# Kernel optimization log

Measured on AMD Instinct MI355X. Metric: run time of the kernel, lower is better.

## Reference

```python
import jax, jax.numpy as jnp
import numpy as np
from jax import lax

B = 1024
D_VQ = 64
KS = 1024
KX = 1024
BETA = 0.25


def _conv1d(x, w, b):
    # x: [N, Cin, L], w: [Cout, Cin, 3], 'same' padding
    y = lax.conv_general_dilated(x, w, (1,), [(1, 1)], dimension_numbers=('NCH', 'OIH', 'NCH'))
    return y + b[None, :, None]


def _conv2d(x, w, b):
    # x: [N, Cin, H, W], w: [Cout, Cin, 3, 3], 'same' padding
    y = lax.conv_general_dilated(x, w, (1, 1), [(1, 1), (1, 1)], dimension_numbers=('NCHW', 'OIHW', 'NCHW'))
    return y + b[None, :, None, None]


def _gelu(x):
    return jax.nn.gelu(x, approximate=False)


def _vq_ema(z_e, codebook, beta):
    # z_e: [N, D], codebook: [K, D]
    d = (jnp.sum(z_e * z_e, axis=1, keepdims=True)
         - 2.0 * (z_e @ codebook.T)
         + jnp.sum(codebook * codebook, axis=1)[None, :])  # [N, K]
    idx = jnp.argmin(d, axis=1)                              # [N]
    z_q = codebook[idx]                                      # gather [N, D]
    vq_loss = beta * jnp.mean((z_e - lax.stop_gradient(z_q)) ** 2)
    z_q_st = z_e + lax.stop_gradient(z_q - z_e)              # straight-through
    n = z_e.shape[0]
    probs = jnp.zeros((codebook.shape[0],), z_e.dtype).at[idx].add(1.0) / n
    perplexity = jnp.exp(-jnp.sum(probs * jnp.log(probs + 1e-10)))
    return z_q_st, idx, vq_loss, perplexity


def setup_inputs() -> dict:
    key = jax.random.key(0)
    ks = iter(jax.random.split(key, 40))

    def p(shape, s=0.05):
        return jax.random.normal(next(ks), shape, jnp.float32) * s

    inp = {
        'cubes': jax.random.normal(next(ks), (B, 9, 8, 72), jnp.float32),
        # spectral encoder
        's_w1': p((16, 1, 3)), 's_b1': jnp.zeros((16,), jnp.float32),
        's_w2': p((16, 16, 3)), 's_b2': jnp.zeros((16,), jnp.float32),
        's_fc_w': p((D_VQ, 16 * 8)), 's_fc_b': jnp.zeros((D_VQ,), jnp.float32),
        'cb_s': p((KS, D_VQ), 1.0),
        # spectral decoder
        's_dec_fc_w': p((16 * 8, D_VQ)), 's_dec_fc_b': jnp.zeros((16 * 8,), jnp.float32),
        's_dec_w1': p((16, 16, 3)), 's_dec_b1': jnp.zeros((16,), jnp.float32),
        's_dec_w2': p((1, 16, 3)), 's_dec_b2': jnp.zeros((1,), jnp.float32),
        # spatial encoder
        'x_w1': p((16, 8, 3, 3)), 'x_b1': jnp.zeros((16,), jnp.float32),
        'x_w2': p((16, 16, 3, 3)), 'x_b2': jnp.zeros((16,), jnp.float32),
        'x_fc_w': p((D_VQ, 16 * 3 * 3)), 'x_fc_b': jnp.zeros((D_VQ,), jnp.float32),
        'cb_x': p((KX, D_VQ), 1.0),
        # spatial decoder
        'x_dec_fc_w': p((16 * 3 * 3, D_VQ)), 'x_dec_fc_b': jnp.zeros((16 * 3 * 3,), jnp.float32),
        'x_dec_w1': p((16, 16, 3, 3)), 'x_dec_b1': jnp.zeros((16,), jnp.float32),
        'x_dec_w2': p((8, 16, 3, 3)), 'x_dec_b2': jnp.zeros((8,), jnp.float32),
        'return_recon': 1,
    }
    return inp


def reference(cubes, s_w1, s_b1, s_w2, s_b2, s_fc_w, s_fc_b, cb_s,
              s_dec_fc_w, s_dec_fc_b, s_dec_w1, s_dec_b1, s_dec_w2, s_dec_b2,
              x_w1, x_b1, x_w2, x_b2, x_fc_w, x_fc_b, cb_x,
              x_dec_fc_w, x_dec_fc_b, x_dec_w1, x_dec_b1, x_dec_w2, x_dec_b2,
              return_recon):
    b, p, t, f = cubes.shape
    n = b * p * t
    c6 = cubes.reshape(b, p, t, 8, 3, 3)                   # [B,P,T,8,3,3]
    cperm = jnp.transpose(c6, (0, 1, 2, 4, 5, 3))          # [B,P,T,3,3,8]

    # --- spectral path ---
    spec = jnp.mean(cperm, axis=(3, 4))                    # [B,P,T,8]
    spec_seq = spec.reshape(n, 1, 8)
    s = _gelu(_conv1d(spec_seq, s_w1, s_b1))
    s = _gelu(_conv1d(s, s_w2, s_b2))
    z_e_s = s.reshape(n, 16 * 8) @ s_fc_w.T + s_fc_b       # [N,D]
    z_q_s, k_idx, vq_loss_s, perplex_s = _vq_ema(z_e_s, cb_s, BETA)
    emb_s = z_q_s.reshape(b, p, t, D_VQ)
    k_idx = k_idx.reshape(b, p, t)

    # --- spatial path ---
    spatial = c6.reshape(n, 8, 3, 3)
    x = _gelu(_conv2d(spatial, x_w1, x_b1))
    x = _gelu(_conv2d(x, x_w2, x_b2))
    z_e_x = x.reshape(n, 16 * 9) @ x_fc_w.T + x_fc_b
    z_q_x, m_idx, vq_loss_x, perplex_x = _vq_ema(z_e_x, cb_x, BETA)
    emb_x = z_q_x.reshape(b, p, t, D_VQ)
    m_idx = m_idx.reshape(b, p, t)

    total = vq_loss_s + vq_loss_x

    if return_recon:
        s_dec = (z_q_s @ s_dec_fc_w.T + s_dec_fc_b).reshape(n, 16, 8)
        s_dec = _gelu(_conv1d(s_dec, s_dec_w1, s_dec_b1))
        recon_s = _conv1d(s_dec, s_dec_w2, s_dec_b2)[:, 0, :].reshape(b, p, t, 8)
        recon_loss_s = jnp.mean((recon_s - spec) ** 2)

        x_dec = (z_q_x @ x_dec_fc_w.T + x_dec_fc_b).reshape(n, 16, 3, 3)
        x_dec = _gelu(_conv2d(x_dec, x_dec_w1, x_dec_b1))
        recon_x = _conv2d(x_dec, x_dec_w2, x_dec_b2)        # [N,8,3,3]
        recon_loss_x = jnp.mean((recon_x - spatial) ** 2)
        recon_loss_total = recon_loss_s + recon_loss_x
    else:
        recon_loss_total = jnp.float32(0.0)

    return (emb_s, emb_x, k_idx, m_idx, total, perplex_s, perplex_x, recon_loss_total)
```

## Files before the change

kernel.cpp:

```cpp
#include <hip/hip_runtime.h>
#include <math.h>

#define NTOK 73728

__device__ __forceinline__ float gelu_f(float x) {
    return 0.5f * x * (1.0f + erff(x * 0.70710678118654752440f));
}

__global__ void __launch_bounds__(256) k_prep(
    const float* __restrict__ cb_s, const float* __restrict__ cb_x,
    double* __restrict__ cn_s, double* __restrict__ cn_x,
    const float* __restrict__ s_dw1, const float* __restrict__ s_db1,
    const float* __restrict__ s_dfcw, const float* __restrict__ s_dfcb,
    float* __restrict__ weffT_s, float* __restrict__ beff_s,
    const float* __restrict__ x_dw1, const float* __restrict__ x_db1,
    const float* __restrict__ x_dfcw, const float* __restrict__ x_dfcb,
    float* __restrict__ weffT_x, float* __restrict__ beff_x,
    const float* __restrict__ s_fcw, float* __restrict__ fcwT_s,
    const float* __restrict__ x_fcw, float* __restrict__ fcwT_x,
    const float* __restrict__ s_w2, float* __restrict__ sw2T,
    const float* __restrict__ x_w1, float* __restrict__ xw1T,
    const float* __restrict__ x_w2, float* __restrict__ xw2T,
    const float* __restrict__ x_dw2, float* __restrict__ xdw2T)
{
    int bid = blockIdx.x, tid = threadIdx.x;
    if (bid < 8) {
        int i = bid * 256 + tid;
        const float* cb = (i < 1024) ? cb_s : cb_x;
        double* cn = (i < 1024) ? cn_s : cn_x;
        int c = i & 1023;
        double s = 0.0;
        for (int k = 0; k < 64; ++k) { double v = (double)cb[c * 64 + k]; s += v * v; }
        cn[c] = s;
    } else if (bid < 40) {
        int idx = (bid - 8) * 256 + tid;
        int o = idx >> 6, d = idx & 63;
        int c = o >> 3, l = o & 7;
        double acc = 0.0;
        for (int ci = 0; ci < 16; ++ci)
            for (int dd = 0; dd < 3; ++dd) {
                int ll = l + dd - 1;
                if (ll < 0 || ll > 7) continue;
                acc += (double)s_dw1[(c * 16 + ci) * 3 + dd] * (double)s_dfcw[(ci * 8 + ll) * 64 + d];
            }
        weffT_s[d * 132 + o] = (float)acc;
        if (o < 4) weffT_s[d * 132 + 128 + o] = 0.f;
        if (d == 0) {
            double bb = (double)s_db1[c];
            for (int ci = 0; ci < 16; ++ci)
                for (int dd = 0; dd < 3; ++dd) {
                    int ll = l + dd - 1;
                    if (ll < 0 || ll > 7) continue;
                    bb += (double)s_dw1[(c * 16 + ci) * 3 + dd] * (double)s_dfcb[ci * 8 + ll];
                }
            beff_s[o] = (float)bb;
        }
    } else if (bid < 76) {
        int idx = (bid - 40) * 256 + tid;
        int o = idx >> 6, d = idx & 63;
        int c = o / 9, p = o - c * 9;
        int i = p / 3, j = p % 3;
        double acc = 0.0;
        for (int ci = 0; ci < 16; ++ci)
            for (int di = 0; di < 3; ++di) {
                int ii = i + di - 1; if (ii < 0 || ii > 2) continue;
                for (int dj = 0; dj < 3; ++dj) {
                    int jj = j + dj - 1; if (jj < 0 || jj > 2) continue;
                    acc += (double)x_dw1[((c * 16 + ci) * 3 + di) * 3 + dj]
                         * (double)x_dfcw[(ci * 9 + ii * 3 + jj) * 64 + d];
                }
            }
        weffT_x[d * 148 + o] = (float)acc;
        if (o < 4) weffT_x[d * 148 + 144 + o] = 0.f;
        if (d == 0) {
            double bb = (double)x_db1[c];
            for (int ci = 0; ci < 16; ++ci)
                for (int di = 0; di < 3; ++di) {
                    int ii = i + di - 1; if (ii < 0 || ii > 2) continue;
                    for (int dj = 0; dj < 3; ++dj) {
                        int jj = j + dj - 1; if (jj < 0 || jj > 2) continue;
                        bb += (double)x_dw1[((c * 16 + ci) * 3 + di) * 3 + dj]
                            * (double)x_dfcb[ci * 9 + ii * 3 + jj];
                    }
                }
            beff_x[o] = (float)bb;
        }
    } else if (bid < 108) {
        int i = (bid - 76) * 256 + tid;
        fcwT_s[i] = s_fcw[(i & 63) * 128 + (i >> 6)];
    } else if (bid < 144) {
        int i = (bid - 108) * 256 + tid;
        fcwT_x[i] = x_fcw[(i & 63) * 144 + (i >> 6)];
    } else {
        int i = (bid - 144) * 256 + tid;
        if (i < 768) {
            int c = i & 15, r = i >> 4;
            int ci = r / 3, dd = r % 3;
            sw2T[i] = s_w2[(c * 16 + ci) * 3 + dd];
        } else if (i < 1920) {
            int j = i - 768;
            int c = j & 15, r = j >> 4;
            int ci = r / 9, tap = r % 9;
            xw1T[j] = x_w1[(c * 8 + ci) * 9 + tap];
        } else if (i < 4224) {
            int j = i - 1920;
            int c = j & 15, r = j >> 4;
            int ci = r / 9, tap = r % 9;
            xw2T[j] = x_w2[(c * 16 + ci) * 9 + tap];
        } else {
            int j = i - 4224;
            int co = j & 7, r = j >> 3;
            int ci = r / 9, tap = r % 9;
            xdw2T[j] = x_dw2[(co * 16 + ci) * 9 + tap];
        }
    }
}

__global__ void __launch_bounds__(256) k_enc(
    const float* __restrict__ cubes,
    const float* __restrict__ s_w1, const float* __restrict__ s_b1,
    const float* __restrict__ sw2T, const float* __restrict__ s_b2,
    const float* __restrict__ fcwT_s, const float* __restrict__ s_fcb,
    float* __restrict__ emb_s,
    const float* __restrict__ xw1T, const float* __restrict__ x_b1,
    const float* __restrict__ xw2T, const float* __restrict__ x_b2,
    const float* __restrict__ fcwT_x, const float* __restrict__ x_fcb,
    float* __restrict__ emb_x)
{
    __shared__ float U[6528];
    int tid = threadIdx.x;
    int t = tid >> 4, c = tid & 15;
    if (blockIdx.x < 4608) {
        int b = blockIdx.x;
        float* S = U;
        float* A = U + 128;
        float* Bb = U + 2304;
        if (tid < 128) {
            int tk = tid >> 3, f = tid & 7;
            const float* cu = cubes + ((size_t)b * 16 + tk) * 72 + f * 9;
            float s = 0.f;
            #pragma unroll
            for (int k = 0; k < 9; ++k) s += cu[k];
            S[tk * 8 + f] = s * (1.0f / 9.0f);
        }
        __syncthreads();
        {
            float s0[8];
            *(float4*)&s0[0] = *(const float4*)&S[t * 8];
            *(float4*)&s0[4] = *(const float4*)&S[t * 8 + 4];
            float wa = s_w1[c * 3 + 0], wb = s_w1[c * 3 + 1], wc = s_w1[c * 3 + 2], bb = s_b1[c];
            #pragma unroll
            for (int l = 0; l < 8; ++l) {
                float v = fmaf(wb, s0[l], bb);
                if (l > 0) v = fmaf(wa, s0[l - 1], v);
                if (l < 7) v = fmaf(wc, s0[l + 1], v);
                A[t * 136 + c * 8 + l] = gelu_f(v);
            }
        }
        __syncthreads();
        {
            float acc[8];
            #pragma unroll
            for (int l = 0; l < 8; ++l) acc[l] = s_b2[c];
            for (int ci = 0; ci < 16; ++ci) {
                float r[8];
                *(float4*)&r[0] = *(const float4*)&A[t * 136 + ci * 8];
                *(float4*)&r[4] = *(const float4*)&A[t * 136 + ci * 8 + 4];
                float wa = sw2T[(ci * 3 + 0) * 16 + c];
                float wb = sw2T[(ci * 3 + 1) * 16 + c];
                float wc = sw2T[(ci * 3 + 2) * 16 + c];
                #pragma unroll
                for (int l = 0; l < 8; ++l) {
                    if (l > 0) acc[l] = fmaf(wa, r[l - 1], acc[l]);
                    acc[l] = fmaf(wb, r[l], acc[l]);
                    if (l < 7) acc[l] = fmaf(wc, r[l + 1], acc[l]);
                }
            }
            #pragma unroll
            for (int l = 0; l < 8; ++l) Bb[t * 136 + c * 8 + l] = gelu_f(acc[l]);
        }
        __syncthreads();
        {
            float4 zv = make_float4(s_fcb[c * 4 + 0], s_fcb[c * 4 + 1], s_fcb[c * 4 + 2], s_fcb[c * 4 + 3]);
            #pragma unroll 4
            for (int e = 0; e < 128; ++e) {
                float be = Bb[t * 136 + e];
                float4 wv = *(const float4*)(fcwT_s + (e << 6) + (c << 2));
                zv.x = fmaf(wv.x, be, zv.x);
                zv.y = fmaf(wv.y, be, zv.y);
                zv.z = fmaf(wv.z, be, zv.z);
                zv.w = fmaf(wv.w, be, zv.w);
            }
            *(float4*)(emb_s + ((size_t)b * 16 + t) * 64 + c * 4) = zv;
        }
    } else {
        int b = blockIdx.x - 4608;
        float* A = U;
        float* Bb = U + 3200;
        for (int u = tid; u < 1152; u += 256) {
            int tk = u / 72, e = u - tk * 72;
            int ci = e / 9, p = e - ci * 9;
            A[tk * 200 + ci * 12 + p] = cubes[(size_t)b * 1152 + u];
        }
        __syncthreads();
        {
            float acc[9];
            #pragma unroll
            for (int p = 0; p < 9; ++p) acc[p] = x_b1[c];
            for (int ci = 0; ci < 8; ++ci) {
                float r[12];
                *(float4*)&r[0] = *(const float4*)&A[t * 200 + ci * 12];
                *(float4*)&r[4] = *(const float4*)&A[t * 200 + ci * 12 + 4];
                *(float4*)&r[8] = *(const float4*)&A[t * 200 + ci * 12 + 8];
                float wv[9];
                #pragma unroll
                for (int q = 0; q < 9; ++q) wv[q] = xw1T[(ci * 9 + q) * 16 + c];
                #pragma unroll
                for (int p = 0; p < 9; ++p) {
                    int i = p / 3, j = p % 3;
                    #pragma unroll
                    for (int di = 0; di < 3; ++di) {
                        int ii = i + di - 1; if (ii < 0 || ii > 2) continue;
                        #pragma unroll
                        for (int dj = 0; dj < 3; ++dj) {
                            int jj = j + dj - 1; if (jj < 0 || jj > 2) continue;
                            acc[p] = fmaf(wv[di * 3 + dj], r[ii * 3 + jj], acc[p]);
                        }
                    }
                }
            }
            #pragma unroll
            for (int p = 0; p < 9; ++p) Bb[t * 200 + c * 12 + p] = gelu_f(acc[p]);
        }
        __syncthreads();
        {
            float acc[9];
            #pragma unroll
            for (int p = 0; p < 9; ++p) acc[p] = x_b2[c];
            for (int ci = 0; ci < 16; ++ci) {
                float r[12];
                *(float4*)&r[0] = *(const float4*)&Bb[t * 200 + ci * 12];
                *(float4*)&r[4] = *(const float4*)&Bb[t * 200 + ci * 12 + 4];
                *(float4*)&r[8] = *(const float4*)&Bb[t * 200 + ci * 12 + 8];
                float wv[9];
                #pragma unroll
                for (int q = 0; q < 9; ++q) wv[q] = xw2T[(ci * 9 + q) * 16 + c];
                #pragma unroll
                for (int p = 0; p < 9; ++p) {
                    int i = p / 3, j = p % 3;
                    #pragma unroll
                    for (int di = 0; di < 3; ++di) {
                        int ii = i + di - 1; if (ii < 0 || ii > 2) continue;
                        #pragma unroll
                        for (int dj = 0; dj < 3; ++dj) {
                            int jj = j + dj - 1; if (jj < 0 || jj > 2) continue;
                            acc[p] = fmaf(wv[di * 3 + dj], r[ii * 3 + jj], acc[p]);
                        }
                    }
                }
            }
            __syncthreads();
            #pragma unroll
            for (int p = 0; p < 9; ++p) A[t * 200 + c * 12 + p] = gelu_f(acc[p]);
        }
        __syncthreads();
        {
            float4 zv = make_float4(x_fcb[c * 4 + 0], x_fcb[c * 4 + 1], x_fcb[c * 4 + 2], x_fcb[c * 4 + 3]);
            #pragma unroll 4
            for (int e = 0; e < 144; ++e) {
                int ci = e / 9, p = e - ci * 9;
                float be = A[t * 200 + ci * 12 + p];
                float4 wv = *(const float4*)(fcwT_x + (e << 6) + (c << 2));
                zv.x = fmaf(wv.x, be, zv.x);
                zv.y = fmaf(wv.y, be, zv.y);
                zv.z = fmaf(wv.z, be, zv.z);
                zv.w = fmaf(wv.w, be, zv.w);
            }
            *(float4*)(emb_x + ((size_t)b * 16 + t) * 64 + c * 4) = zv;
        }
    }
}

__global__ void __launch_bounds__(256) k_vq(
    float* __restrict__ emb_s, float* __restrict__ emb_x,
    const float* __restrict__ cb_s, const float* __restrict__ cb_x,
    const double* __restrict__ cn_s, const double* __restrict__ cn_x,
    float* __restrict__ kidx, float* __restrict__ midx,
    int* __restrict__ hist_s, int* __restrict__ hist_x,
    double* __restrict__ p_vq_s, double* __restrict__ p_vq_x)
{
    __shared__ double pbest[4][64];
    __shared__ int pidx[4][64];
    __shared__ int lh[1024];
    int blk = blockIdx.x;
    int path = (blk >= 1152) ? 1 : 0;
    int b = blk - (path << 10) - (path << 7);
    float* emb = path ? emb_x : emb_s;
    const float* cb = path ? cb_x : cb_s;
    const double* cn = path ? cn_x : cn_s;
    float* idx_out = path ? midx : kidx;
    int* hist = path ? hist_x : hist_s;
    double* partial = path ? p_vq_x : p_vq_s;

    int tid = threadIdx.x;
    int w = tid >> 6, l = tid & 63;
    for (int u = tid; u < 1024; u += 256) lh[u] = 0;
    size_t n = (size_t)b * 64 + l;
    float z[64];
    {
        const float4* zp = (const float4*)(emb + n * 64);
        #pragma unroll
        for (int k = 0; k < 16; ++k) *(float4*)&z[k * 4] = zp[k];
    }
    int base = __builtin_amdgcn_readfirstlane(w << 8);
    const float* crb = cb + ((size_t)base << 6);
    const double* cnb = cn + base;
    double best = 1e300; int bi = base;
    for (int cc = 0; cc < 256; ++cc) {
        const float* cr = crb + (cc << 6);
        float d0 = 0.f, d1 = 0.f, d2 = 0.f, d3 = 0.f;
        #pragma unroll
        for (int k = 0; k < 64; k += 4) {
            d0 = fmaf(z[k + 0], cr[k + 0], d0);
            d1 = fmaf(z[k + 1], cr[k + 1], d1);
            d2 = fmaf(z[k + 2], cr[k + 2], d2);
            d3 = fmaf(z[k + 3], cr[k + 3], d3);
        }
        float dot = (d0 + d1) + (d2 + d3);
        double dd = cnb[cc] - 2.0 * (double)dot;
        if (dd < best) { best = dd; bi = base + cc; }
    }
    pbest[w][l] = best; pidx[w][l] = bi;
    __syncthreads();
    if (w == 0) {
        double bB = pbest[0][l]; int bj = pidx[0][l];
        #pragma unroll
        for (int q = 1; q < 4; ++q) {
            double d = pbest[q][l];
            if (d < bB) { bB = d; bj = pidx[q][l]; }
        }
        idx_out[n] = (float)bj;
        float qv[64];
        {
            const float4* cq = (const float4*)(cb + ((size_t)bj << 6));
            #pragma unroll
            for (int k = 0; k < 16; ++k) *(float4*)&qv[k * 4] = cq[k];
        }
        float vs = 0.f;
        #pragma unroll
        for (int k = 0; k < 64; ++k) { float df = z[k] - qv[k]; vs = fmaf(df, df, vs); }
        float4* zo = (float4*)(emb + n * 64);
        #pragma unroll
        for (int k = 0; k < 16; ++k) zo[k] = *(float4*)&qv[k * 4];
        atomicAdd(&lh[bj], 1);
        double s = (double)vs;
        #pragma unroll
        for (int o = 32; o > 0; o >>= 1) s += __shfl_down(s, o);
        if (l == 0) partial[b] = s;
    }
    __syncthreads();
    for (int u = tid; u < 1024; u += 256) if (lh[u] > 0) atomicAdd(&hist[u], lh[u]);
}

__global__ void __launch_bounds__(256) k_dec(
    const float* __restrict__ emb_s, const float* __restrict__ emb_x,
    const float* __restrict__ cubes,
    const float* __restrict__ weffT_s, const float* __restrict__ beff_s,
    const float* __restrict__ s_dw2, const float* __restrict__ s_db2,
    const float* __restrict__ weffT_x, const float* __restrict__ beff_x,
    const float* __restrict__ xdw2T, const float* __restrict__ x_db2,
    double* __restrict__ p_rec_s, double* __restrict__ p_rec_x)
{
    __shared__ float U[6016];
    __shared__ double wred[4];
    int tid = threadIdx.x;
    int t = tid >> 4, c = tid & 15;
    if (blockIdx.x < 4608) {
        int b = blockIdx.x;
        float* Z = U;
        float* Bb = U + 1152;
        float* S = U + 3328;
        {
            int tk = tid >> 4, dq = tid & 15;
            *(float4*)&Z[tk * 72 + dq * 4] =
                *(const float4*)(emb_s + (size_t)b * 1024 + (size_t)tid * 4);
        }
        if (tid < 128) {
            int tk = tid >> 3, f = tid & 7;
            const float* cu = cubes + ((size_t)b * 16 + tk) * 72 + f * 9;
            float s = 0.f;
            #pragma unroll
            for (int k = 0; k < 9; ++k) s += cu[k];
            S[tk * 8 + f] = s * (1.0f / 9.0f);
        }
        __syncthreads();
        {
            float4 a0 = make_float4(0.f, 0.f, 0.f, 0.f);
            float4 a1 = make_float4(0.f, 0.f, 0.f, 0.f);
            #pragma unroll 8
            for (int k = 0; k < 64; ++k) {
                float zk = Z[t * 72 + k];
                float4 w0 = *(const float4*)(weffT_s + k * 132 + (c << 2));
                float4 w1v = *(const float4*)(weffT_s + k * 132 + 64 + (c << 2));
                a0.x = fmaf(w0.x, zk, a0.x); a0.y = fmaf(w0.y, zk, a0.y);
                a0.z = fmaf(w0.z, zk, a0.z); a0.w = fmaf(w0.w, zk, a0.w);
                a1.x = fmaf(w1v.x, zk, a1.x); a1.y = fmaf(w1v.y, zk, a1.y);
                a1.z = fmaf(w1v.z, zk, a1.z); a1.w = fmaf(w1v.w, zk, a1.w);
            }
            int o0 = c << 2, o1 = 64 + (c << 2);
            float4 g0 = make_float4(gelu_f(a0.x + beff_s[o0 + 0]), gelu_f(a0.y + beff_s[o0 + 1]),
                                    gelu_f(a0.z + beff_s[o0 + 2]), gelu_f(a0.w + beff_s[o0 + 3]));
            float4 g1 = make_float4(gelu_f(a1.x + beff_s[o1 + 0]), gelu_f(a1.y + beff_s[o1 + 1]),
                                    gelu_f(a1.z + beff_s[o1 + 2]), gelu_f(a1.w + beff_s[o1 + 3]));
            *(float4*)&Bb[t * 136 + o0] = g0;
            *(float4*)&Bb[t * 136 + o1] = g1;
        }
        __syncthreads();
        float acc2 = 0.f;
        {
            int h = c >> 3, pos = c & 7;
            float a = (h == 0) ? s_db2[0] : 0.f;
            for (int ci = h * 8; ci < h * 8 + 8; ++ci) {
                const float* w = s_dw2 + ci * 3;
                const float* hb = &Bb[t * 136 + ci * 8];
                if (pos > 0) a = fmaf(w[0], hb[pos - 1], a);
                a = fmaf(w[1], hb[pos], a);
                if (pos < 7) a = fmaf(w[2], hb[pos + 1], a);
            }
            a += __shfl_xor(a, 8);
            if (h == 0) { float df = a - S[t * 8 + pos]; acc2 = df * df; }
        }
        double s = (double)acc2;
        #pragma unroll
        for (int o = 32; o > 0; o >>= 1) s += __shfl_down(s, o);
        if ((tid & 63) == 0) wred[tid >> 6] = s;
        __syncthreads();
        if (tid == 0) p_rec_s[b] = wred[0] + wred[1] + wred[2] + wred[3];
    } else {
        int b = blockIdx.x - 4608;
        float* Z = U;
        float* H = U + 1152;
        float* T = U + 4352;
        {
            int tk = tid >> 4, dq = tid & 15;
            *(float4*)&Z[tk * 72 + dq * 4] =
                *(const float4*)(emb_x + (size_t)b * 1024 + (size_t)tid * 4);
        }
        for (int u = tid; u < 1152; u += 256) {
            int tk = u / 72, e = u - tk * 72;
            int ci = e / 9, p = e - ci * 9;
            T[tk * 104 + ci * 12 + p] = cubes[(size_t)b * 1152 + u];
        }
        __syncthreads();
        {
            float4 a0 = make_float4(0.f, 0.f, 0.f, 0.f);
            float4 a1 = make_float4(0.f, 0.f, 0.f, 0.f);
            float4 a2 = make_float4(0.f, 0.f, 0.f, 0.f);
            #pragma unroll 8
            for (int k = 0; k < 64; ++k) {
                float zk = Z[t * 72 + k];
                float4 w0 = *(const float4*)(weffT_x + k * 148 + (c << 2));
                float4 w1v = *(const float4*)(weffT_x + k * 148 + 64 + (c << 2));
                float4 w2v = *(const float4*)(weffT_x + k * 148 + 128 + (c << 2));
                a0.x = fmaf(w0.x, zk, a0.x); a0.y = fmaf(w0.y, zk, a0.y);
                a0.z = fmaf(w0.z, zk, a0.z); a0.w = fmaf(w0.w, zk, a0.w);
                a1.x = fmaf(w1v.x, zk, a1.x); a1.y = fmaf(w1v.y, zk, a1.y);
                a1.z = fmaf(w1v.z, zk, a1.z); a1.w = fmaf(w1v.w, zk, a1.w);
                a2.x = fmaf(w2v.x, zk, a2.x); a2.y = fmaf(w2v.y, zk, a2.y);
                a2.z = fmaf(w2v.z, zk, a2.z); a2.w = fmaf(w2v.w, zk, a2.w);
            }
            float av[12] = {a0.x, a0.y, a0.z, a0.w, a1.x, a1.y, a1.z, a1.w, a2.x, a2.y, a2.z, a2.w};
            #pragma unroll
            for (int q = 0; q < 12; ++q) {
                int o = (c << 2) + ((q >> 2) << 6) + (q & 3);
                int ch = o / 9, p = o - ch * 9;
                H[t * 200 + ch * 12 + p] = gelu_f(av[q] + beff_x[o]);
            }
        }
        __syncthreads();
        float acc2 = 0.f;
        {
            int co = c >> 1, h = c & 1;
            float accp[9];
            #pragma unroll
            for (int p = 0; p < 9; ++p) accp[p] = (h == 0) ? x_db2[co] : 0.f;
            for (int ci = h * 8; ci < h * 8 + 8; ++ci) {
                float r[12];
                *(float4*)&r[0] = *(const float4*)&H[t * 200 + ci * 12];
                *(float4*)&r[4] = *(const float4*)&H[t * 200 + ci * 12 + 4];
                *(float4*)&r[8] = *(const float4*)&H[t * 200 + ci * 12 + 8];
                float wv[9];
                #pragma unroll
                for (int q = 0; q < 9; ++q) wv[q] = xdw2T[(ci * 9 + q) * 8 + co];
                #pragma unroll
                for (int p = 0; p < 9; ++p) {
                    int i = p / 3, j = p % 3;
                    #pragma unroll
                    for (int di = 0; di < 3; ++di) {
                        int ii = i + di - 1; if (ii < 0 || ii > 2) continue;
                        #pragma unroll
                        for (int dj = 0; dj < 3; ++dj) {
                            int jj = j + dj - 1; if (jj < 0 || jj > 2) continue;
                            accp[p] = fmaf(wv[di * 3 + dj], r[ii * 3 + jj], accp[p]);
                        }
                    }
                }
            }
            #pragma unroll
            for (int p = 0; p < 9; ++p) {
                float tot = accp[p] + __shfl_xor(accp[p], 1);
                if (h == 0) { float df = tot - T[t * 104 + co * 12 + p]; acc2 = fmaf(df, df, acc2); }
            }
        }
        double s = (double)acc2;
        #pragma unroll
        for (int o = 32; o > 0; o >>= 1) s += __shfl_down(s, o);
        if ((tid & 63) == 0) wred[tid >> 6] = s;
        __syncthreads();
        if (tid == 0) p_rec_x[b] = wred[0] + wred[1] + wred[2] + wred[3];
    }
}

__global__ void __launch_bounds__(256) k_final(
    const double* __restrict__ p_vq_s, const double* __restrict__ p_vq_x,
    const double* __restrict__ p_rec_s, const double* __restrict__ p_rec_x,
    const int* __restrict__ hist_s, const int* __restrict__ hist_x,
    const int* __restrict__ rr,
    float* __restrict__ outscal)
{
    __shared__ double wred[4];
    int tid = threadIdx.x;
    auto bred = [&](double v) -> double {
        #pragma unroll
        for (int o = 32; o > 0; o >>= 1) v += __shfl_down(v, o);
        __syncthreads();
        if ((tid & 63) == 0) wred[tid >> 6] = v;
        __syncthreads();
        return wred[0] + wred[1] + wred[2] + wred[3];
    };
    double a;
    a = 0; for (int t = tid; t < 1152; t += 256) a += p_vq_s[t];
    double vq_s = bred(a);
    a = 0; for (int t = tid; t < 1152; t += 256) a += p_vq_x[t];
    double vq_x = bred(a);
    a = 0; for (int t = tid; t < 4608; t += 256) a += p_rec_s[t];
    double rec_s = bred(a);
    a = 0; for (int t = tid; t < 4608; t += 256) a += p_rec_x[t];
    double rec_x = bred(a);
    a = 0;
    for (int t = tid; t < 1024; t += 256) {
        double cnt = (double)hist_s[t];
        if (cnt > 0.0) { double p = cnt / (double)NTOK; a += p * log(p + 1e-10); }
    }
    double ent_s = bred(a);
    a = 0;
    for (int t = tid; t < 1024; t += 256) {
        double cnt = (double)hist_x[t];
        if (cnt > 0.0) { double p = cnt / (double)NTOK; a += p * log(p + 1e-10); }
    }
    double ent_x = bred(a);
    if (tid == 0) {
        double total = 0.25 * (vq_s / 4718592.0 + vq_x / 4718592.0);
        double rec = (rr[0] != 0) ? (rec_s / 589824.0 + rec_x / 5308416.0) : 0.0;
        outscal[0] = (float)total;
        outscal[1] = (float)exp(-ent_s);
        outscal[2] = (float)exp(-ent_x);
        outscal[3] = (float)rec;
    }
}

extern "C" void kernel_launch(void* const* d_in, const int* in_sizes, int n_in,
                              void* d_out, int out_size, void* d_ws, size_t ws_size,
                              hipStream_t stream)
{
    const float* cubes  = (const float*)d_in[0];
    const float* s_w1   = (const float*)d_in[1];
    const float* s_b1   = (const float*)d_in[2];
    const float* s_w2   = (const float*)d_in[3];
    const float* s_b2   = (const float*)d_in[4];
    const float* s_fcw  = (const float*)d_in[5];
    const float* s_fcb  = (const float*)d_in[6];
    const float* cb_s   = (const float*)d_in[7];
    const float* s_dfcw = (const float*)d_in[8];
    const float* s_dfcb = (const float*)d_in[9];
    const float* s_dw1  = (const float*)d_in[10];
    const float* s_db1  = (const float*)d_in[11];
    const float* s_dw2  = (const float*)d_in[12];
    const float* s_db2  = (const float*)d_in[13];
    const float* x_w1   = (const float*)d_in[14];
    const float* x_b1   = (const float*)d_in[15];
    const float* x_w2   = (const float*)d_in[16];
    const float* x_b2   = (const float*)d_in[17];
    const float* x_fcw  = (const float*)d_in[18];
    const float* x_fcb  = (const float*)d_in[19];
    const float* cb_x   = (const float*)d_in[20];
    const float* x_dfcw = (const float*)d_in[21];
    const float* x_dfcb = (const float*)d_in[22];
    const float* x_dw1  = (const float*)d_in[23];
    const float* x_db1  = (const float*)d_in[24];
    const float* x_dw2  = (const float*)d_in[25];
    const float* x_db2  = (const float*)d_in[26];
    const int*   rr     = (const int*)d_in[27];

    float* out   = (float*)d_out;
    float* emb_s = out;
    float* emb_x = out + 4718592;
    float* kidx  = out + 9437184;
    float* midx  = out + 9510912;
    float* scal  = out + 9584640;

    char* ws = (char*)d_ws;
    int*    hist_s  = (int*)(ws + 0);
    int*    hist_x  = (int*)(ws + 4096);
    double* cn_s    = (double*)(ws + 8192);
    double* cn_x    = (double*)(ws + 16384);
    double* p_vq_s  = (double*)(ws + 24576);
    double* p_vq_x  = (double*)(ws + 33792);
    double* p_rec_s = (double*)(ws + 43008);
    double* p_rec_x = (double*)(ws + 79872);
    float*  beff_s  = (float*)(ws + 116736);
    float*  beff_x  = (float*)(ws + 117248);
    float*  weffT_s = (float*)(ws + 117824);
    float*  weffT_x = (float*)(ws + 151616);
    float*  fcwT_s  = (float*)(ws + 189504);
    float*  fcwT_x  = (float*)(ws + 222272);
    float*  sw2T    = (float*)(ws + 259136);
    float*  xw1T    = (float*)(ws + 262208);
    float*  xw2T    = (float*)(ws + 266816);
    float*  xdw2T   = (float*)(ws + 276032);

    hipMemsetAsync(d_ws, 0, 8192, stream);
    k_prep<<<165, 256, 0, stream>>>(cb_s, cb_x, cn_s, cn_x,
                                    s_dw1, s_db1, s_dfcw, s_dfcb, weffT_s, beff_s,
                                    x_dw1, x_db1, x_dfcw, x_dfcb, weffT_x, beff_x,
                                    s_fcw, fcwT_s, x_fcw, fcwT_x,
                                    s_w2, sw2T, x_w1, xw1T, x_w2, xw2T, x_dw2, xdw2T);
    k_enc<<<9216, 256, 0, stream>>>(cubes, s_w1, s_b1, sw2T, s_b2, fcwT_s, s_fcb, emb_s,
                                    xw1T, x_b1, xw2T, x_b2, fcwT_x, x_fcb, emb_x);
    k_vq<<<2304, 256, 0, stream>>>(emb_s, emb_x, cb_s, cb_x, cn_s, cn_x,
                                   kidx, midx, hist_s, hist_x, p_vq_s, p_vq_x);
    k_dec<<<9216, 256, 0, stream>>>(emb_s, emb_x, cubes,
                                    weffT_s, beff_s, s_dw2, s_db2,
                                    weffT_x, beff_x, xdw2T, x_db2,
                                    p_rec_s, p_rec_x);
    k_final<<<1, 256, 0, stream>>>(p_vq_s, p_vq_x, p_rec_s, p_rec_x, hist_s, hist_x, rr, scal);
}
```

Before: 883.1 us.

## Give each VQ thread a full codebook scan instead of splitting codes across waves

The VQ kernel now assigns 256 tokens per block, one per thread, and each thread scans all 1024 codes. Previously four waves split the codebook for the same 64 tokens and merged through shared memory. This removes the cross-wave merge and lets all four waves do the gather, write and loss work, and it cuts the grid from 2304 to 576 blocks. The cost is four times the serial loop length per thread and fewer blocks to spread across the CUs. The four waves now read different tokens, so the per-code codebook rows are no longer shared by the whole block.

After: 993.5 us. 1.12x slower.

```diff
diff --git a/kernel.cpp b/kernel.cpp
--- a/kernel.cpp
+++ b/kernel.cpp
@@ -289,12 +289,11 @@
     int* __restrict__ hist_s, int* __restrict__ hist_x,
     double* __restrict__ p_vq_s, double* __restrict__ p_vq_x)
 {
-    __shared__ double pbest[4][64];
-    __shared__ int pidx[4][64];
     __shared__ int lh[1024];
+    __shared__ double wred[4];
     int blk = blockIdx.x;
-    int path = (blk >= 1152) ? 1 : 0;
-    int b = blk - (path << 10) - (path << 7);
+    int path = (blk >= 288) ? 1 : 0;
+    int b = blk - path * 288;
     float* emb = path ? emb_x : emb_s;
     const float* cb = path ? cb_x : cb_s;
     const double* cn = path ? cn_x : cn_s;
@@ -305,19 +304,17 @@
     int tid = threadIdx.x;
     int w = tid >> 6, l = tid & 63;
     for (int u = tid; u < 1024; u += 256) lh[u] = 0;
-    size_t n = (size_t)b * 64 + l;
+    __syncthreads();
+    size_t n = (size_t)b * 256 + (w << 6) + l;
     float z[64];
     {
         const float4* zp = (const float4*)(emb + n * 64);
         #pragma unroll
         for (int k = 0; k < 16; ++k) *(float4*)&z[k * 4] = zp[k];
     }
-    int base = __builtin_amdgcn_readfirstlane(w << 8);
-    const float* crb = cb + ((size_t)base << 6);
-    const double* cnb = cn + base;
-    double best = 1e300; int bi = base;
-    for (int cc = 0; cc < 256; ++cc) {
-        const float* cr = crb + (cc << 6);
+    double best = 1e300; int bi = 0;
+    for (int cc = 0; cc < 1024; ++cc) {
+        const float* cr = cb + ((size_t)cc << 6);
         float d0 = 0.f, d1 = 0.f, d2 = 0.f, d3 = 0.f;
         #pragma unroll
         for (int k = 0; k < 64; k += 4) {
@@ -327,38 +324,29 @@
             d3 = fmaf(z[k + 3], cr[k + 3], d3);
         }
         float dot = (d0 + d1) + (d2 + d3);
-        double dd = cnb[cc] - 2.0 * (double)dot;
-        if (dd < best) { best = dd; bi = base + cc; }
-    }
-    pbest[w][l] = best; pidx[w][l] = bi;
+        double dd = cn[cc] - 2.0 * (double)dot;
+        if (dd < best) { best = dd; bi = cc; }
+    }
+    idx_out[n] = (float)bi;
+    float qv[64];
+    {
+        const float4* cq = (const float4*)(cb + ((size_t)bi << 6));
+        #pragma unroll
+        for (int k = 0; k < 16; ++k) *(float4*)&qv[k * 4] = cq[k];
+    }
+    float vs = 0.f;
+    #pragma unroll
+    for (int k = 0; k < 64; ++k) { float df = z[k] - qv[k]; vs = fmaf(df, df, vs); }
+    float4* zo = (float4*)(emb + n * 64);
+    #pragma unroll
+    for (int k = 0; k < 16; ++k) zo[k] = *(float4*)&qv[k * 4];
+    atomicAdd(&lh[bi], 1);
+    double s = (double)vs;
+    #pragma unroll
+    for (int o = 32; o > 0; o >>= 1) s += __shfl_down(s, o);
+    if (l == 0) wred[w] = s;
     __syncthreads();
-    if (w == 0) {
-        double bB = pbest[0][l]; int bj = pidx[0][l];
-        #pragma unroll
-        for (int q = 1; q < 4; ++q) {
-            double d = pbest[q][l];
-            if (d < bB) { bB = d; bj = pidx[q][l]; }
-        }
-        idx_out[n] = (float)bj;
-        float qv[64];
-        {
-            const float4* cq = (const float4*)(cb + ((size_t)bj << 6));
-            #pragma unroll
-            for (int k = 0; k < 16; ++k) *(float4*)&qv[k * 4] = cq[k];
-        }
-        float vs = 0.f;
-        #pragma unroll
-        for (int k = 0; k < 64; ++k) { float df = z[k] - qv[k]; vs = fmaf(df, df, vs); }
-        float4* zo = (float4*)(emb + n * 64);
-        #pragma unroll
-        for (int k = 0; k < 16; ++k) zo[k] = *(float4*)&qv[k * 4];
-        atomicAdd(&lh[bj], 1);
-        double s = (double)vs;
-        #pragma unroll
-        for (int o = 32; o > 0; o >>= 1) s += __shfl_down(s, o);
-        if (l == 0) partial[b] = s;
-    }
-    __syncthreads();
+    if (tid == 0) partial[b] = wred[0] + wred[1] + wred[2] + wred[3];
     for (int u = tid; u < 1024; u += 256) if (lh[u] > 0) atomicAdd(&hist[u], lh[u]);
 }
 
@@ -539,9 +527,9 @@
         return wred[0] + wred[1] + wred[2] + wred[3];
     };
     double a;
-    a = 0; for (int t = tid; t < 1152; t += 256) a += p_vq_s[t];
+    a = 0; for (int t = tid; t < 288; t += 256) a += p_vq_s[t];
     double vq_s = bred(a);
-    a = 0; for (int t = tid; t < 1152; t += 256) a += p_vq_x[t];
+    a = 0; for (int t = tid; t < 288; t += 256) a += p_vq_x[t];
     double vq_x = bred(a);
     a = 0; for (int t = tid; t < 4608; t += 256) a += p_rec_s[t];
     double rec_s = bred(a);
@@ -637,8 +625,8 @@
                                     s_w2, sw2T, x_w1, xw1T, x_w2, xw2T, x_dw2, xdw2T);
     k_enc<<<9216, 256, 0, stream>>>(cubes, s_w1, s_b1, sw2T, s_b2, fcwT_s, s_fcb, emb_s,
                                     xw1T, x_b1, xw2T, x_b2, fcwT_x, x_fcb, emb_x);
-    k_vq<<<2304, 256, 0, stream>>>(emb_s, emb_x, cb_s, cb_x, cn_s, cn_x,
-                                   kidx, midx, hist_s, hist_x, p_vq_s, p_vq_x);
+    k_vq<<<576, 256, 0, stream>>>(emb_s, emb_x, cb_s, cb_x, cn_s, cn_x,
+                                  kidx, midx, hist_s, hist_x, p_vq_s, p_vq_x);
     k_dec<<<9216, 256, 0, stream>>>(emb_s, emb_x, cubes,
                                     weffT_s, beff_s, s_dw2, s_db2,
                                     weffT_x, beff_x, xdw2T, x_db2,
```

## Use fp16 dot2 codebook search with top-2 margin and fp64 rescoring fallback

Applied to the files above, without the earlier changes.

The VQ nearest-codebook search now runs on an fp16 copy of the codebooks using packed dot2 instructions and fp32 distances, and keeps the best and second-best candidates per token. Tokens whose top-2 gap is below a norm-scaled margin are rescored exactly in fp64 across the full codebook, with the work spread over the wavefront. This cuts the cost of the dominant distance loop (half the codebook bytes, packed math, no fp64 compare) while aiming to keep argmin results exact. The margin heuristic could miss a true nearest code when fp16 error exceeds it, and the rescoring path adds divergence and extra loads.

Result: slower. 1.110 ms (+25.7%).

```diff
diff --git a/kernel.cpp b/kernel.cpp
--- a/kernel.cpp
+++ b/kernel.cpp
@@ -2,14 +2,28 @@
 #include <math.h>
 
 #define NTOK 73728
+
+typedef __fp16 h2 __attribute__((ext_vector_type(2)));
+union U32H2 { unsigned u; h2 h; };
 
 __device__ __forceinline__ float gelu_f(float x) {
     return 0.5f * x * (1.0f + erff(x * 0.70710678118654752440f));
 }
 
+__device__ __forceinline__ float dot2f(h2 a, h2 b, float acc) {
+#if __has_builtin(__builtin_amdgcn_fdot2)
+    return __builtin_amdgcn_fdot2(a, b, acc, false);
+#else
+    acc = fmaf((float)a[0], (float)b[0], acc);
+    return fmaf((float)a[1], (float)b[1], acc);
+#endif
+}
+
 __global__ void __launch_bounds__(256) k_prep(
     const float* __restrict__ cb_s, const float* __restrict__ cb_x,
     double* __restrict__ cn_s, double* __restrict__ cn_x,
+    float* __restrict__ cnf_s, float* __restrict__ cnf_x,
+    __fp16* __restrict__ cbh_s, __fp16* __restrict__ cbh_x,
     const float* __restrict__ s_dw1, const float* __restrict__ s_db1,
     const float* __restrict__ s_dfcw, const float* __restrict__ s_dfcb,
     float* __restrict__ weffT_s, float* __restrict__ beff_s,
@@ -28,10 +42,17 @@
         int i = bid * 256 + tid;
         const float* cb = (i < 1024) ? cb_s : cb_x;
         double* cn = (i < 1024) ? cn_s : cn_x;
+        float* cnf = (i < 1024) ? cnf_s : cnf_x;
+        __fp16* cbh = (i < 1024) ? cbh_s : cbh_x;
         int c = i & 1023;
         double s = 0.0;
-        for (int k = 0; k < 64; ++k) { double v = (double)cb[c * 64 + k]; s += v * v; }
+        for (int k = 0; k < 64; ++k) {
+            float v = cb[c * 64 + k];
+            s += (double)v * (double)v;
+            cbh[c * 64 + k] = (__fp16)v;
+        }
         cn[c] = s;
+        cnf[c] = (float)s;
     } else if (bid < 40) {
         int idx = (bid - 8) * 256 + tid;
         int o = idx >> 6, d = idx & 63;
@@ -284,20 +305,25 @@
 __global__ void __launch_bounds__(256) k_vq(
     float* __restrict__ emb_s, float* __restrict__ emb_x,
     const float* __restrict__ cb_s, const float* __restrict__ cb_x,
+    const unsigned* __restrict__ cbh_s, const unsigned* __restrict__ cbh_x,
     const double* __restrict__ cn_s, const double* __restrict__ cn_x,
+    const float* __restrict__ cnf_s, const float* __restrict__ cnf_x,
     float* __restrict__ kidx, float* __restrict__ midx,
     int* __restrict__ hist_s, int* __restrict__ hist_x,
     double* __restrict__ p_vq_s, double* __restrict__ p_vq_x)
 {
-    __shared__ double pbest[4][64];
-    __shared__ int pidx[4][64];
+    __shared__ float pb1[4][64];
+    __shared__ float pb2[4][64];
+    __shared__ int   pi1[4][64];
     __shared__ int lh[1024];
     int blk = blockIdx.x;
     int path = (blk >= 1152) ? 1 : 0;
     int b = blk - (path << 10) - (path << 7);
     float* emb = path ? emb_x : emb_s;
     const float* cb = path ? cb_x : cb_s;
+    const unsigned* cbh = path ? cbh_x : cbh_s;
     const double* cn = path ? cn_x : cn_s;
+    const float* cnf = path ? cnf_x : cnf_s;
     float* idx_out = path ? midx : kidx;
     int* hist = path ? hist_x : hist_s;
     double* partial = path ? p_vq_x : p_vq_s;
@@ -306,43 +332,86 @@
     int w = tid >> 6, l = tid & 63;
     for (int u = tid; u < 1024; u += 256) lh[u] = 0;
     size_t n = (size_t)b * 64 + l;
-    float z[64];
+    h2 zh[32];
+    float zn2 = 0.f;
     {
         const float4* zp = (const float4*)(emb + n * 64);
         #pragma unroll
-        for (int k = 0; k < 16; ++k) *(float4*)&z[k * 4] = zp[k];
+        for (int k = 0; k < 16; ++k) {
+            float4 v = zp[k];
+            zn2 = fmaf(v.x, v.x, zn2); zn2 = fmaf(v.y, v.y, zn2);
+            zn2 = fmaf(v.z, v.z, zn2); zn2 = fmaf(v.w, v.w, zn2);
+            zh[2 * k + 0] = __builtin_amdgcn_cvt_pkrtz(v.x, v.y);
+            zh[2 * k + 1] = __builtin_amdgcn_cvt_pkrtz(v.z, v.w);
+        }
     }
     int base = __builtin_amdgcn_readfirstlane(w << 8);
-    const float* crb = cb + ((size_t)base << 6);
-    const double* cnb = cn + base;
-    double best = 1e300; int bi = base;
+    const unsigned* crb = cbh + ((size_t)base << 5);
+    const float* cnfb = cnf + base;
+    float b1 = 1e30f, b2v = 1e30f; int i1 = base;
     for (int cc = 0; cc < 256; ++cc) {
-        const float* cr = crb + (cc << 6);
+        const unsigned* cr = crb + (cc << 5);
         float d0 = 0.f, d1 = 0.f, d2 = 0.f, d3 = 0.f;
         #pragma unroll
-        for (int k = 0; k < 64; k += 4) {
-            d0 = fmaf(z[k + 0], cr[k + 0], d0);
-            d1 = fmaf(z[k + 1], cr[k + 1], d1);
-            d2 = fmaf(z[k + 2], cr[k + 2], d2);
-            d3 = fmaf(z[k + 3], cr[k + 3], d3);
+        for (int k = 0; k < 32; k += 4) {
+            U32H2 c0, c1, c2, c3;
+            c0.u = cr[k + 0]; c1.u = cr[k + 1]; c2.u = cr[k + 2]; c3.u = cr[k + 3];
+            d0 = dot2f(zh[k + 0], c0.h, d0);
+            d1 = dot2f(zh[k + 1], c1.h, d1);
+            d2 = dot2f(zh[k + 2], c2.h, d2);
+            d3 = dot2f(zh[k + 3], c3.h, d3);
         }
         float dot = (d0 + d1) + (d2 + d3);
-        double dd = cnb[cc] - 2.0 * (double)dot;
-        if (dd < best) { best = dd; bi = base + cc; }
-    }
-    pbest[w][l] = best; pidx[w][l] = bi;
+        float dd = fmaf(-2.0f, dot, cnfb[cc]);
+        if (dd < b1) { b2v = b1; b1 = dd; i1 = base + cc; }
+        else if (dd < b2v) b2v = dd;
+    }
+    pb1[w][l] = b1; pb2[w][l] = b2v; pi1[w][l] = i1;
     __syncthreads();
     if (w == 0) {
-        double bB = pbest[0][l]; int bj = pidx[0][l];
+        b1 = pb1[0][l]; b2v = pb2[0][l]; i1 = pi1[0][l];
         #pragma unroll
         for (int q = 1; q < 4; ++q) {
-            double d = pbest[q][l];
-            if (d < bB) { bB = d; bj = pidx[q][l]; }
-        }
-        idx_out[n] = (float)bj;
+            float a1 = pb1[q][l], a2 = pb2[q][l];
+            if (a1 < b1) { b2v = fminf(b1, a2); b1 = a1; i1 = pi1[q][l]; }
+            else b2v = fminf(b2v, a1);
+        }
+        float margin = 0.05f * sqrtf(zn2) + 1e-3f;
+        int flag = (b2v - b1 < margin) ? 1 : 0;
+        unsigned long long mask = __ballot(flag != 0);
+        while (mask) {
+            int tk = __ffsll((long long)mask) - 1; mask &= (mask - 1);
+            size_t ntk = (size_t)b * 64 + tk;
+            const float* zt = emb + ntk * 64;
+            double bd = 1e300; int bl = 0;
+            for (int cc2 = 0; cc2 < 16; ++cc2) {
+                int cidx = l * 16 + cc2;
+                const float* cr = cb + ((size_t)cidx << 6);
+                double dot = 0.0;
+                #pragma unroll
+                for (int k = 0; k < 64; ++k)
+                    dot = fma((double)zt[k], (double)cr[k], dot);
+                double dd = cn[cidx] - 2.0 * dot;
+                if (dd < bd) { bd = dd; bl = cidx; }
+            }
+            #pragma unroll
+            for (int m = 1; m < 64; m <<= 1) {
+                double ob = __shfl_xor(bd, m);
+                int oi = __shfl_xor(bl, m);
+                if (ob < bd || (ob == bd && oi < bl)) { bd = ob; bl = oi; }
+            }
+            if (l == tk) i1 = bl;
+        }
+        idx_out[n] = (float)i1;
+        float z[64];
+        {
+            const float4* zp = (const float4*)(emb + n * 64);
+            #pragma unroll
+            for (int k = 0; k < 16; ++k) *(float4*)&z[k * 4] = zp[k];
+        }
         float qv[64];
         {
-            const float4* cq = (const float4*)(cb + ((size_t)bj << 6));
+            const float4* cq = (const float4*)(cb + ((size_t)i1 << 6));
             #pragma unroll
             for (int k = 0; k < 16; ++k) *(float4*)&qv[k * 4] = cq[k];
         }
@@ -352,7 +421,7 @@
         float4* zo = (float4*)(emb + n * 64);
         #pragma unroll
         for (int k = 0; k < 16; ++k) zo[k] = *(float4*)&qv[k * 4];
-        atomicAdd(&lh[bj], 1);
+        atomicAdd(&lh[i1], 1);
         double s = (double)vs;
         #pragma unroll
         for (int o = 32; o > 0; o >>= 1) s += __shfl_down(s, o);
@@ -628,16 +697,22 @@
     float*  xw1T    = (float*)(ws + 262208);
     float*  xw2T    = (float*)(ws + 266816);
     float*  xdw2T   = (float*)(ws + 276032);
+    float*  cnf_s   = (float*)(ws + 280640);
+    float*  cnf_x   = (float*)(ws + 284736);
+    __fp16* cbh_s   = (__fp16*)(ws + 289024);
+    __fp16* cbh_x   = (__fp16*)(ws + 420096);
 
     hipMemsetAsync(d_ws, 0, 8192, stream);
-    k_prep<<<165, 256, 0, stream>>>(cb_s, cb_x, cn_s, cn_x,
+    k_prep<<<165, 256, 0, stream>>>(cb_s, cb_x, cn_s, cn_x, cnf_s, cnf_x, cbh_s, cbh_x,
                                     s_dw1, s_db1, s_dfcw, s_dfcb, weffT_s, beff_s,
                                     x_dw1, x_db1, x_dfcw, x_dfcb, weffT_x, beff_x,
                                     s_fcw, fcwT_s, x_fcw, fcwT_x,
                                     s_w2, sw2T, x_w1, xw1T, x_w2, xw2T, x_dw2, xdw2T);
     k_enc<<<9216, 256, 0, stream>>>(cubes, s_w1, s_b1, sw2T, s_b2, fcwT_s, s_fcb, emb_s,
                                     xw1T, x_b1, xw2T, x_b2, fcwT_x, x_fcb, emb_x);
-    k_vq<<<2304, 256, 0, stream>>>(emb_s, emb_x, cb_s, cb_x, cn_s, cn_x,
+    k_vq<<<2304, 256, 0, stream>>>(emb_s, emb_x, cb_s, cb_x,
+                                   (const unsigned*)cbh_s, (const unsigned*)cbh_x,
+                                   cn_s, cn_x, cnf_s, cnf_x,
                                    kidx, midx, hist_s, hist_x, p_vq_s, p_vq_x);
     k_dec<<<9216, 256, 0, stream>>>(emb_s, emb_x, cubes,
                                     weffT_s, beff_s, s_dw2, s_db2,
```
